# Kernel optimization log

Hardware: AMD Instinct MI355X
Metric: run time of the kernel (lower is better)

The kernel has to match this reference:

```python
import jax, jax.numpy as jnp
import numpy as np

B, LQ, LKV = 2, 2048, 2048
DQ, DKV, HID, NH = 1024, 1024, 1024, 16
HD = HID // NH
EPS = 1e-5


def setup_inputs() -> dict:
    key = jax.random.key(0)
    ks = jax.random.split(key, 12)
    s_q = 1.0 / np.sqrt(DQ)
    s_kv = 1.0 / np.sqrt(DKV)
    s_h = 1.0 / np.sqrt(HID)
    return {
        "query": jax.random.normal(ks[0], (B, LQ, DQ), jnp.float32),
        "key_value": jax.random.normal(ks[1], (B, LKV, DKV), jnp.float32),
        "Wq": jax.random.uniform(ks[2], (DQ, HID), jnp.float32, -s_q, s_q),
        "bq": jax.random.uniform(ks[3], (HID,), jnp.float32, -s_q, s_q),
        "Wk": jax.random.uniform(ks[4], (DKV, HID), jnp.float32, -s_kv, s_kv),
        "bk": jax.random.uniform(ks[5], (HID,), jnp.float32, -s_kv, s_kv),
        "Wv": jax.random.uniform(ks[6], (DKV, HID), jnp.float32, -s_kv, s_kv),
        "bv": jax.random.uniform(ks[7], (HID,), jnp.float32, -s_kv, s_kv),
        "Wo": jax.random.uniform(ks[8], (HID, DQ), jnp.float32, -s_h, s_h),
        "bo": jax.random.uniform(ks[9], (DQ,), jnp.float32, -s_h, s_h),
        "ln_gamma": jnp.ones((DQ,), jnp.float32),
        "ln_beta": jnp.zeros((DQ,), jnp.float32),
    }


def reference(query, key_value, Wq, bq, Wk, bk, Wv, bv, Wo, bo, ln_gamma, ln_beta):
    b, lq, _ = query.shape
    lkv = key_value.shape[1]
    # projections -> [b, heads, len, head_dim]
    Q = (query @ Wq + bq).reshape(b, lq, NH, HD).transpose(0, 2, 1, 3)
    K = (key_value @ Wk + bk).reshape(b, lkv, NH, HD).transpose(0, 2, 1, 3)
    V = (key_value @ Wv + bv).reshape(b, lkv, NH, HD).transpose(0, 2, 1, 3)
    scores = jnp.einsum("bhqd,bhkd->bhqk", Q, K) / jnp.sqrt(jnp.float32(HD))
    attn = jax.nn.softmax(scores, axis=-1)
    ctx = jnp.einsum("bhqk,bhkd->bhqd", attn, V)
    ctx = ctx.transpose(0, 2, 1, 3).reshape(b, lq, HID)
    out = ctx @ Wo + bo
    x = query + out
    mu = jnp.mean(x, axis=-1, keepdims=True)
    var = jnp.mean(jnp.square(x - mu), axis=-1, keepdims=True)
    return (x - mu) / jnp.sqrt(var + EPS) * ln_gamma + ln_beta
```

## Files before the change

kernel.cpp:

```cpp
#include <hip/hip_runtime.h>

typedef unsigned short u16;
typedef __bf16 bf16x8 __attribute__((ext_vector_type(8)));
typedef float f32x4 __attribute__((ext_vector_type(4)));
typedef unsigned short u16x4 __attribute__((ext_vector_type(4)));

#define LOG2E 1.44269504088896340736f
#define LDK 1040
#define LDV 2080
#define EXPM16 12599160.0f

__device__ __forceinline__ u16 f2bf(float f) {
  unsigned u = __float_as_uint(f);
  u += 0x7FFFu + ((u >> 16) & 1u);
  return (u16)(u >> 16);
}

__device__ __forceinline__ void load_lds16(const void* g, void* l) {
  __builtin_amdgcn_global_load_lds(
      (__attribute__((address_space(1))) void*)g,
      (__attribute__((address_space(3))) void*)l, 16, 0, 0);
}

__device__ __forceinline__ f32x4 mfma16(bf16x8 a, bf16x8 b, f32x4 c) {
  return __builtin_amdgcn_mfma_f32_16x16x32_bf16(a, b, c, 0, 0, 0);
}

__global__ __launch_bounds__(256) void pre_kernel(
    const float* __restrict__ q, const float* __restrict__ kv,
    u16* __restrict__ Xq, u16* __restrict__ Xkv,
    const float* __restrict__ Wq, const float* __restrict__ Wk,
    const float* __restrict__ Wv, const float* __restrict__ Wo,
    u16* __restrict__ Wqt, u16* __restrict__ Wkt,
    u16* __restrict__ Wvt, u16* __restrict__ Wot) {
  __shared__ float tile[32][33];
  const int bid = blockIdx.x;
  if (bid < 8192) {
    const int n4each = 4096 * 256;
    int i = bid * 256 + threadIdx.x;
    const float* src; u16* dst; int j;
    if (i < n4each) { src = q; dst = Xq; j = i; }
    else            { src = kv; dst = Xkv; j = i - n4each; }
    const float4 v = ((const float4*)src)[j];
    u16x4 o;
    o.x = f2bf(v.x); o.y = f2bf(v.y); o.z = f2bf(v.z); o.w = f2bf(v.w);
    ((u16x4*)dst)[j] = o;
    return;
  }
  const int t = bid - 8192;
  const int z = t >> 10, rem = t & 1023;
  const float* W; u16* Wt;
  switch (z) {
    case 0: W = Wq; Wt = Wqt; break;
    case 1: W = Wk; Wt = Wkt; break;
    case 2: W = Wv; Wt = Wvt; break;
    default: W = Wo; Wt = Wot; break;
  }
  const int tx = threadIdx.x & 31, ty = threadIdx.x >> 5;
  const int n0 = (rem & 31) * 32, k0 = (rem >> 5) * 32;
#pragma unroll
  for (int i = 0; i < 4; i++)
    tile[ty + i * 8][tx] = W[(size_t)(k0 + ty + i * 8) * 1024 + n0 + tx];
  __syncthreads();
#pragma unroll
  for (int i = 0; i < 4; i++)
    Wt[(size_t)(n0 + ty + i * 8) * 1024 + k0 + tx] = f2bf(tile[tx][ty + i * 8]);
}

__device__ __forceinline__ void gemm_tile(
    const u16* __restrict__ A, int lda, const u16* __restrict__ Bt, int ldb,
    const float* __restrict__ bias, bool brow, float scale,
    u16* __restrict__ Cb, float* __restrict__ Cf,
    int ldc, int bm, int bn, int K) {
  __shared__ alignas(16) u16 As[2][128 * 32];
  __shared__ alignas(16) u16 Bs[2][128 * 32];
  const int tid = threadIdx.x;
  const int wave = tid >> 6, lane = tid & 63;
  const int lm = lane & 15, kq = lane >> 4;
  const int g1 = tid, g2 = tid + 256;
  const u16* Ag1 = A + (size_t)(bm + (g1 >> 2)) * lda + (g1 & 3) * 8;
  const u16* Ag2 = A + (size_t)(bm + (g2 >> 2)) * lda + (g2 & 3) * 8;
  const u16* Bg1 = Bt + (size_t)(bn + (g1 >> 2)) * ldb + (g1 & 3) * 8;
  const u16* Bg2 = Bt + (size_t)(bn + (g2 >> 2)) * ldb + (g2 & 3) * 8;
  const int wm = (wave >> 1) * 64, wn = (wave & 1) * 64;

  load_lds16(Ag1, &As[0][g1 * 8]);
  load_lds16(Ag2, &As[0][g2 * 8]);
  load_lds16(Bg1, &Bs[0][g1 * 8]);
  load_lds16(Bg2, &Bs[0][g2 * 8]);

  f32x4 acc[4][4] = {};
  int cur = 0;
  for (int k0 = 0; k0 < K; k0 += 32) {
    if (k0 + 32 < K) {
      const int nxt = cur ^ 1;
      load_lds16(Ag1 + k0 + 32, &As[nxt][g1 * 8]);
      load_lds16(Ag2 + k0 + 32, &As[nxt][g2 * 8]);
      load_lds16(Bg1 + k0 + 32, &Bs[nxt][g1 * 8]);
      load_lds16(Bg2 + k0 + 32, &Bs[nxt][g2 * 8]);
      __builtin_amdgcn_sched_barrier(0);
      asm volatile("s_waitcnt vmcnt(4)" ::: "memory");
    } else {
      __builtin_amdgcn_sched_barrier(0);
      asm volatile("s_waitcnt vmcnt(0)" ::: "memory");
    }
    __builtin_amdgcn_sched_barrier(0);
    __builtin_amdgcn_s_barrier();

    __builtin_amdgcn_s_setprio(1);
    bf16x8 a[4], b[4];
#pragma unroll
    for (int t = 0; t < 4; t++)
      a[t] = *(const bf16x8*)&As[cur][(wm + t * 16 + lm) * 32 + kq * 8];
#pragma unroll
    for (int t = 0; t < 4; t++)
      b[t] = *(const bf16x8*)&Bs[cur][(wn + t * 16 + lm) * 32 + kq * 8];
#pragma unroll
    for (int mt = 0; mt < 4; mt++)
#pragma unroll
      for (int nt = 0; nt < 4; nt++)
        acc[mt][nt] = mfma16(a[mt], b[nt], acc[mt][nt]);
    __builtin_amdgcn_s_setprio(0);
    __builtin_amdgcn_sched_barrier(0);
    __builtin_amdgcn_s_barrier();
    cur ^= 1;
  }
#pragma unroll
  for (int mt = 0; mt < 4; mt++) {
    float rb[4];
#pragma unroll
    for (int r = 0; r < 4; r++)
      rb[r] = (bias && brow) ? bias[bm + wm + mt * 16 + kq * 4 + r] : 0.f;
#pragma unroll
    for (int nt = 0; nt < 4; nt++) {
      const int col = bn + wn + nt * 16 + lm;
      const float cb = (bias && !brow) ? bias[col] : 0.f;
#pragma unroll
      for (int r = 0; r < 4; r++) {
        const int row = bm + wm + mt * 16 + kq * 4 + r;
        const size_t idx = (size_t)row * ldc + col;
        const float v = (acc[mt][nt][r] + rb[r] + cb) * scale;
        if (Cf) Cf[idx] = v;
        else    Cb[idx] = f2bf(v);
      }
    }
  }
}

__global__ __launch_bounds__(256) void proj_gemm_kernel(
    const u16* __restrict__ Xq, const u16* __restrict__ Xkv,
    const u16* __restrict__ Wqt, const u16* __restrict__ Wkt, const u16* __restrict__ Wvt,
    const float* __restrict__ bq, const float* __restrict__ bk, const float* __restrict__ bv,
    u16* __restrict__ Qp, u16* __restrict__ Kp, u16* __restrict__ Vt, float qscale) {
  const int bid = blockIdx.x;
  const u16 *A, *Bt; const float* bias; u16* C;
  bool brow = false; float sc = 1.f; int ldc = 1024; int bm, bn;
  if (bid < 512) {
    const int r = bid & 255;
    const int xcd = r & 7, s = r >> 3;
    bm = (xcd * 4 + (s >> 3)) * 128;
    bn = (s & 7) * 128;
    if (bid < 256) { A = Xq;  Bt = Wqt; bias = bq; C = Qp; sc = qscale; }
    else           { A = Xkv; Bt = Wkt; bias = bk; C = Kp; ldc = LDK;  }
  } else {
    int r = bid - 512;
    const int z = r >> 7; r &= 127;
    const int xcd = r & 7, s = r >> 3;
    bm = (s >> 1) * 128;
    bn = (xcd * 2 + (s & 1)) * 128;
    A = Wvt; Bt = Xkv + (size_t)z * 2048 * 1024; bias = bv; brow = true;
    C = Vt + (size_t)z * 1024 * LDV; ldc = LDV;
  }
  gemm_tile(A, 1024, Bt, 1024, bias, brow, sc, C, nullptr, ldc, bm, bn, 1024);
}

__global__ __launch_bounds__(256) void ogemm_kernel(
    const u16* __restrict__ Ctx, const u16* __restrict__ Wot,
    float* __restrict__ X0, float* __restrict__ X1) {
  const int z = blockIdx.z;
  float* Cf = z ? X1 : X0;
  const int lin = blockIdx.x + 8 * blockIdx.y;
  const int xcd = lin & 7, s = lin >> 3;
  const int bm = (xcd * 4 + (s >> 3)) * 128, bn = (s & 7) * 128;
  gemm_tile(Ctx + z * 512, 1024, Wot + z * 512, 1024, nullptr, false, 1.f,
            nullptr, Cf, 1024, bm, bn, 512);
}

__global__ __launch_bounds__(512, 4) void attn_kernel(
    const u16* __restrict__ Qp, const u16* __restrict__ Kp,
    const u16* __restrict__ Vt, u16* __restrict__ ctx) {
  __shared__ alignas(16) u16 smem[32768];
  const int tid = threadIdx.x;
  const int wave = tid >> 6, lane = tid & 63;
  const int kh = wave >> 2, w4 = wave & 3;
  const int lm = lane & 15, kq = lane >> 4;
  const int L = blockIdx.x;
  const int xcd = L & 7, s = L >> 3;
  const int combo = xcd + 8 * (s >> 4);
  const int qb = s & 15;
  const int h = combo & 15, b = combo >> 4;
  const int qbase = qb * 128 + w4 * 32;

  u16* Ksh = smem + kh * 8192;
  u16* Vsh = smem + 16384 + kh * 8192;

  bf16x8 qf[2][2];
#pragma unroll
  for (int qt = 0; qt < 2; qt++)
#pragma unroll
    for (int kc = 0; kc < 2; kc++)
      qf[qt][kc] = *(const bf16x8*)(Qp + (size_t)(b * 2048 + qbase + qt * 16 + lm) * 1024 +
                                    h * 64 + kc * 32 + kq * 8);

  union { u16 u[8]; bf16x8 v; } uo;
#pragma unroll
  for (int i = 0; i < 8; i++) uo.u[i] = 0x3F80;
  const bf16x8 ones = uo.v;

  const u16* Kb = Kp + ((size_t)b * 2048 + kh * 1024) * LDK + h * 64;
  const u16* Vb = Vt + (size_t)(b * 1024 + h * 64) * LDV + kh * 1024;
  const int sp = lane ^ ((lane >> 3) & 7);
  const int c4 = sp >> 2, c3 = sp & 3;
  const int kvsw = ((lm * 4 + kq) ^ (lm >> 1)) * 8;

  f32x4 o[4][2] = {};
  f32x4 lsum[2] = {};

#pragma unroll
  for (int j = 0; j < 2; j++) {
    const int ii = w4 * 2 + j;
    const u16* gk = Kb + (size_t)(16 * (ii & 3) + c4) * LDK + (ii >> 2) * 32 + c3 * 8;
    load_lds16(gk, &Ksh[ii * 512 + lane * 8]);
    const u16* gv = Vb + (size_t)(16 * (ii & 3) + c4) * LDV + (ii >> 2) * 32 + c3 * 8;
    load_lds16(gv, &Vsh[ii * 512 + lane * 8]);
  }

  int cur = 0;
  for (int t = 0; t < 16; ++t) {
    if (t < 15) {
      const int kvn = (t + 1) * 64;
      const int nb = (cur ^ 1) * 4096;
#pragma unroll
      for (int j = 0; j < 2; j++) {
        const int ii = w4 * 2 + j;
        const u16* gk = Kb + (size_t)(kvn + 16 * (ii & 3) + c4) * LDK + (ii >> 2) * 32 + c3 * 8;
        load_lds16(gk, &Ksh[nb + ii * 512 + lane * 8]);
        const u16* gv = Vb + (size_t)(16 * (ii & 3) + c4) * LDV + kvn + (ii >> 2) * 32 + c3 * 8;
        load_lds16(gv, &Vsh[nb + ii * 512 + lane * 8]);
      }
      __builtin_amdgcn_sched_barrier(0);
      asm volatile("s_waitcnt vmcnt(4)" ::: "memory");
    } else {
      __builtin_amdgcn_sched_barrier(0);
      asm volatile("s_waitcnt vmcnt(0)" ::: "memory");
    }
    __builtin_amdgcn_sched_barrier(0);
    __builtin_amdgcn_s_barrier();

    const int cb = cur * 4096;
    __builtin_amdgcn_s_setprio(1);

    bf16x8 kf[2][4];
#pragma unroll
    for (int kc = 0; kc < 2; kc++)
#pragma unroll
      for (int kvt = 0; kvt < 4; kvt++)
        kf[kc][kvt] = *(const bf16x8*)&Ksh[cb + kc * 2048 + kvt * 512 + kvsw];

    bf16x8 pf[2][2];
#pragma unroll
    for (int qt = 0; qt < 2; qt++) {
      f32x4 st[4] = {};
#pragma unroll
      for (int kc = 0; kc < 2; kc++)
#pragma unroll
        for (int kvt = 0; kvt < 4; kvt++)
          st[kvt] = mfma16(kf[kc][kvt], qf[qt][kc], st[kvt]);
      unsigned Xd[4][2];
#pragma unroll
      for (int kvt = 0; kvt < 4; kvt++) {
        const unsigned e0 = __float_as_uint(fmaf(st[kvt][0], 128.f, EXPM16));
        const unsigned e1 = __float_as_uint(fmaf(st[kvt][1], 128.f, EXPM16));
        const unsigned e2 = __float_as_uint(fmaf(st[kvt][2], 128.f, EXPM16));
        const unsigned e3 = __float_as_uint(fmaf(st[kvt][3], 128.f, EXPM16));
        Xd[kvt][0] = __builtin_amdgcn_perm(e1, e0, 0x05040100u);
        Xd[kvt][1] = __builtin_amdgcn_perm(e3, e2, 0x05040100u);
      }
#pragma unroll
      for (int K1 = 0; K1 < 2; K1++) {
        unsigned a0 = Xd[2 * K1][0], b0 = Xd[2 * K1 + 1][0];
        unsigned a1 = Xd[2 * K1][1], b1 = Xd[2 * K1 + 1][1];
        asm("v_permlane32_swap_b32 %0, %1\n\t"
            "v_permlane16_swap_b32 %0, %1"
            : "+v"(a0), "+v"(b0));
        asm("v_permlane32_swap_b32 %0, %1\n\t"
            "v_permlane16_swap_b32 %0, %1"
            : "+v"(a1), "+v"(b1));
        union { uint4 u; bf16x8 v; } c;
        c.u.x = a0; c.u.y = a1; c.u.z = b0; c.u.w = b1;
        pf[qt][K1] = c.v;
      }
    }
#pragma unroll
    for (int s2 = 0; s2 < 2; s2++) {
      bf16x8 vf[4];
#pragma unroll
      for (int hdt = 0; hdt < 4; hdt++)
        vf[hdt] = *(const bf16x8*)&Vsh[cb + s2 * 2048 + hdt * 512 + kvsw];
#pragma unroll
      for (int qt = 0; qt < 2; qt++) {
        lsum[qt] = mfma16(ones, pf[qt][s2], lsum[qt]);
#pragma unroll
        for (int hdt = 0; hdt < 4; hdt++)
          o[hdt][qt] = mfma16(vf[hdt], pf[qt][s2], o[hdt][qt]);
      }
    }
    __builtin_amdgcn_s_setprio(0);
    __builtin_amdgcn_sched_barrier(0);
    __builtin_amdgcn_s_barrier();
    cur ^= 1;
  }

  __syncthreads();
  float* ex = (float*)smem;
  const int exi = (w4 * 64 + lane) * 36;
  if (kh == 1) {
#pragma unroll
    for (int qt = 0; qt < 2; qt++)
#pragma unroll
      for (int hdt = 0; hdt < 4; hdt++)
        *(f32x4*)&ex[exi + (qt * 4 + hdt) * 4] = o[hdt][qt];
    ex[exi + 32] = lsum[0][0];
    ex[exi + 33] = lsum[1][0];
  }
  __syncthreads();
  if (kh == 0) {
#pragma unroll
    for (int qt = 0; qt < 2; qt++) {
      const float lo = ex[exi + 32 + qt];
      const float rl = 1.f / (lsum[qt][0] + lo);
      u16* cbp = ctx + (size_t)(b * 2048 + qbase + qt * 16 + lm) * 1024 + h * 64 + kq * 4;
#pragma unroll
      for (int hdt = 0; hdt < 4; hdt++) {
        const f32x4 op = *(const f32x4*)&ex[exi + (qt * 4 + hdt) * 4];
        u16x4 w;
#pragma unroll
        for (int r = 0; r < 4; r++) w[r] = f2bf((o[hdt][qt][r] + op[r]) * rl);
        *(u16x4*)(cbp + hdt * 16) = w;
      }
    }
  }
}

__global__ __launch_bounds__(256) void ln_kernel(
    const float* __restrict__ x0, const float* __restrict__ x1,
    const float* __restrict__ q, const float* __restrict__ bo,
    const float* __restrict__ gamma, const float* __restrict__ beta,
    float* __restrict__ out) {
  const int row = blockIdx.x;
  const int t = threadIdx.x;
  const size_t g = (size_t)row * 256 + t;
  const float4 a = ((const float4*)x0)[g];
  const float4 c = ((const float4*)x1)[g];
  const float4 d = ((const float4*)q)[g];
  const float4 bv = ((const float4*)bo)[t];
  float4 v;
  v.x = a.x + c.x + d.x + bv.x;
  v.y = a.y + c.y + d.y + bv.y;
  v.z = a.z + c.z + d.z + bv.z;
  v.w = a.w + c.w + d.w + bv.w;
  float s = v.x + v.y + v.z + v.w;
  float s2 = v.x * v.x + v.y * v.y + v.z * v.z + v.w * v.w;
#pragma unroll
  for (int m = 1; m < 64; m <<= 1) {
    s += __shfl_xor(s, m);
    s2 += __shfl_xor(s2, m);
  }
  __shared__ float red[8];
  const int wave = t >> 6, lane = t & 63;
  if (lane == 0) { red[wave] = s; red[4 + wave] = s2; }
  __syncthreads();
  s = red[0] + red[1] + red[2] + red[3];
  s2 = red[4] + red[5] + red[6] + red[7];
  const float mu = s * (1.f / 1024.f);
  const float var = s2 * (1.f / 1024.f) - mu * mu;
  const float rstd = rsqrtf(var + 1e-5f);
  const float4 gm = ((const float4*)gamma)[t];
  const float4 bt = ((const float4*)beta)[t];
  float4 o;
  o.x = (v.x - mu) * rstd * gm.x + bt.x;
  o.y = (v.y - mu) * rstd * gm.y + bt.y;
  o.z = (v.z - mu) * rstd * gm.z + bt.z;
  o.w = (v.w - mu) * rstd * gm.w + bt.w;
  ((float4*)(out + (size_t)row * 1024))[t] = o;
}

extern "C" void kernel_launch(void* const* d_in, const int* in_sizes, int n_in,
                              void* d_out, int out_size, void* d_ws, size_t ws_size,
                              hipStream_t stream) {
  const float* query     = (const float*)d_in[0];
  const float* key_value = (const float*)d_in[1];
  const float* Wq = (const float*)d_in[2];
  const float* bq = (const float*)d_in[3];
  const float* Wk = (const float*)d_in[4];
  const float* bk = (const float*)d_in[5];
  const float* Wv = (const float*)d_in[6];
  const float* bv = (const float*)d_in[7];
  const float* Wo = (const float*)d_in[8];
  const float* bo = (const float*)d_in[9];
  const float* gamma = (const float*)d_in[10];
  const float* beta  = (const float*)d_in[11];
  float* out = (float*)d_out;

  const size_t MT = (size_t)4096 * 1024;
  const size_t WT = (size_t)1024 * 1024;
  char* ws = (char*)d_ws;
  u16* Xq  = (u16*)ws; ws += MT * 2;
  u16* Xkv = (u16*)ws; ws += MT * 2;
  u16* Wqt = (u16*)ws; ws += WT * 2;
  u16* Wkt = (u16*)ws; ws += WT * 2;
  u16* Wvt = (u16*)ws; ws += WT * 2;
  u16* Wot = (u16*)ws; ws += WT * 2;
  u16* Qp  = (u16*)ws; ws += MT * 2;
  u16* Kp  = (u16*)ws; ws += (size_t)4096 * LDK * 2;
  u16* Vt  = (u16*)ws; ws += (size_t)2048 * LDV * 2;
  float* X0 = (float*)ws; ws += MT * 4;
  float* X1 = (float*)ws; ws += MT * 4;
  u16* Ctx = Xq;

  const float qscale = 0.125f * LOG2E;

  pre_kernel<<<12288, 256, 0, stream>>>(query, key_value, Xq, Xkv,
                                        Wq, Wk, Wv, Wo, Wqt, Wkt, Wvt, Wot);
  proj_gemm_kernel<<<768, 256, 0, stream>>>(Xq, Xkv, Wqt, Wkt, Wvt, bq, bk, bv,
                                            Qp, Kp, Vt, qscale);
  attn_kernel<<<512, 512, 0, stream>>>(Qp, Kp, Vt, Ctx);
  ogemm_kernel<<<dim3(8, 32, 2), 256, 0, stream>>>(Ctx, Wot, X0, X1);
  ln_kernel<<<4096, 256, 0, stream>>>(X0, X1, query, bo, gamma, beta, out);
}
```

Before: 213.5 us.

## Swizzle GEMM LDS layout and replace split-K output GEMM with 64x128 tiles

The shared GEMM tile now loads global data into a swizzled LDS layout and reads it back with matching XOR-swizzled offsets, aimed at removing LDS bank conflicts on the MFMA fragment reads. The output projection drops its two-way split-K, which wrote two fp32 partial buffers. It becomes a dedicated kernel with 64x128 tiles over the full K=1024, 512 blocks, writing one buffer. The layernorm then reads one partial instead of two, cutting fp32 traffic at the cost of a longer K loop per block.

```diff
diff --git a/kernel.cpp b/kernel.cpp
--- a/kernel.cpp
+++ b/kernel.cpp
@@ -77,12 +77,15 @@
   const int tid = threadIdx.x;
   const int wave = tid >> 6, lane = tid & 63;
   const int lm = lane & 15, kq = lane >> 4;
+  const int sp = lane ^ ((lane >> 3) & 7);
+  const int r4 = sp >> 2, q3 = sp & 3;
   const int g1 = tid, g2 = tid + 256;
-  const u16* Ag1 = A + (size_t)(bm + (g1 >> 2)) * lda + (g1 & 3) * 8;
-  const u16* Ag2 = A + (size_t)(bm + (g2 >> 2)) * lda + (g2 & 3) * 8;
-  const u16* Bg1 = Bt + (size_t)(bn + (g1 >> 2)) * ldb + (g1 & 3) * 8;
-  const u16* Bg2 = Bt + (size_t)(bn + (g2 >> 2)) * ldb + (g2 & 3) * 8;
+  const u16* Ag1 = A + (size_t)(bm + wave * 16 + r4) * lda + q3 * 8;
+  const u16* Ag2 = A + (size_t)(bm + 64 + wave * 16 + r4) * lda + q3 * 8;
+  const u16* Bg1 = Bt + (size_t)(bn + wave * 16 + r4) * ldb + q3 * 8;
+  const u16* Bg2 = Bt + (size_t)(bn + 64 + wave * 16 + r4) * ldb + q3 * 8;
   const int wm = (wave >> 1) * 64, wn = (wave & 1) * 64;
+  const int kvsw = ((lm * 4 + kq) ^ (lm >> 1)) * 8;
 
   load_lds16(Ag1, &As[0][g1 * 8]);
   load_lds16(Ag2, &As[0][g2 * 8]);
@@ -111,10 +114,10 @@
     bf16x8 a[4], b[4];
 #pragma unroll
     for (int t = 0; t < 4; t++)
-      a[t] = *(const bf16x8*)&As[cur][(wm + t * 16 + lm) * 32 + kq * 8];
+      a[t] = *(const bf16x8*)&As[cur][((wm >> 4) + t) * 512 + kvsw];
 #pragma unroll
     for (int t = 0; t < 4; t++)
-      b[t] = *(const bf16x8*)&Bs[cur][(wn + t * 16 + lm) * 32 + kq * 8];
+      b[t] = *(const bf16x8*)&Bs[cur][((wn >> 4) + t) * 512 + kvsw];
 #pragma unroll
     for (int mt = 0; mt < 4; mt++)
 #pragma unroll
@@ -176,14 +179,75 @@
 
 __global__ __launch_bounds__(256) void ogemm_kernel(
     const u16* __restrict__ Ctx, const u16* __restrict__ Wot,
-    float* __restrict__ X0, float* __restrict__ X1) {
-  const int z = blockIdx.z;
-  float* Cf = z ? X1 : X0;
-  const int lin = blockIdx.x + 8 * blockIdx.y;
+    float* __restrict__ X) {
+  __shared__ alignas(16) u16 As[2][64 * 32];
+  __shared__ alignas(16) u16 Bs[2][128 * 32];
+  const int tid = threadIdx.x;
+  const int wave = tid >> 6, lane = tid & 63;
+  const int lm = lane & 15, kq = lane >> 4;
+  const int lin = blockIdx.x;
   const int xcd = lin & 7, s = lin >> 3;
-  const int bm = (xcd * 4 + (s >> 3)) * 128, bn = (s & 7) * 128;
-  gemm_tile(Ctx + z * 512, 1024, Wot + z * 512, 1024, nullptr, false, 1.f,
-            nullptr, Cf, 1024, bm, bn, 512);
+  const int bm = (xcd * 8 + (s >> 3)) * 64;
+  const int bn = (s & 7) * 128;
+  const int sp = lane ^ ((lane >> 3) & 7);
+  const int r4 = sp >> 2, q3 = sp & 3;
+  const int g1 = tid, g2 = tid + 256;
+  const u16* Ag  = Ctx + (size_t)(bm + wave * 16 + r4) * 1024 + q3 * 8;
+  const u16* Bg1 = Wot + (size_t)(bn + wave * 16 + r4) * 1024 + q3 * 8;
+  const u16* Bg2 = Wot + (size_t)(bn + 64 + wave * 16 + r4) * 1024 + q3 * 8;
+  const int wn = wave * 32;
+  const int kvsw = ((lm * 4 + kq) ^ (lm >> 1)) * 8;
+
+  load_lds16(Ag,  &As[0][g1 * 8]);
+  load_lds16(Bg1, &Bs[0][g1 * 8]);
+  load_lds16(Bg2, &Bs[0][g2 * 8]);
+
+  f32x4 acc[4][2] = {};
+  int cur = 0;
+  for (int k0 = 0; k0 < 1024; k0 += 32) {
+    if (k0 + 32 < 1024) {
+      const int nxt = cur ^ 1;
+      load_lds16(Ag + k0 + 32,  &As[nxt][g1 * 8]);
+      load_lds16(Bg1 + k0 + 32, &Bs[nxt][g1 * 8]);
+      load_lds16(Bg2 + k0 + 32, &Bs[nxt][g2 * 8]);
+      __builtin_amdgcn_sched_barrier(0);
+      asm volatile("s_waitcnt vmcnt(3)" ::: "memory");
+    } else {
+      __builtin_amdgcn_sched_barrier(0);
+      asm volatile("s_waitcnt vmcnt(0)" ::: "memory");
+    }
+    __builtin_amdgcn_sched_barrier(0);
+    __builtin_amdgcn_s_barrier();
+
+    __builtin_amdgcn_s_setprio(1);
+    bf16x8 a[4], b[2];
+#pragma unroll
+    for (int t = 0; t < 4; t++)
+      a[t] = *(const bf16x8*)&As[cur][t * 512 + kvsw];
+#pragma unroll
+    for (int t = 0; t < 2; t++)
+      b[t] = *(const bf16x8*)&Bs[cur][((wn >> 4) + t) * 512 + kvsw];
+#pragma unroll
+    for (int mt = 0; mt < 4; mt++)
+#pragma unroll
+      for (int nt = 0; nt < 2; nt++)
+        acc[mt][nt] = mfma16(a[mt], b[nt], acc[mt][nt]);
+    __builtin_amdgcn_s_setprio(0);
+    __builtin_amdgcn_sched_barrier(0);
+    __builtin_amdgcn_s_barrier();
+    cur ^= 1;
+  }
+#pragma unroll
+  for (int mt = 0; mt < 4; mt++)
+#pragma unroll
+    for (int nt = 0; nt < 2; nt++) {
+      const int col = bn + wn + nt * 16 + lm;
+#pragma unroll
+      for (int r = 0; r < 4; r++) {
+        const int row = bm + mt * 16 + kq * 4 + r;
+        X[(size_t)row * 1024 + col] = acc[mt][nt][r];
+      }
+    }
 }
 
 __global__ __launch_bounds__(512, 4) void attn_kernel(
@@ -353,7 +417,7 @@
 }
 
 __global__ __launch_bounds__(256) void ln_kernel(
-    const float* __restrict__ x0, const float* __restrict__ x1,
+    const float* __restrict__ x0,
     const float* __restrict__ q, const float* __restrict__ bo,
     const float* __restrict__ gamma, const float* __restrict__ beta,
     float* __restrict__ out) {
@@ -361,14 +425,13 @@
   const int t = threadIdx.x;
   const size_t g = (size_t)row * 256 + t;
   const float4 a = ((const float4*)x0)[g];
-  const float4 c = ((const float4*)x1)[g];
   const float4 d = ((const float4*)q)[g];
   const float4 bv = ((const float4*)bo)[t];
   float4 v;
-  v.x = a.x + c.x + d.x + bv.x;
-  v.y = a.y + c.y + d.y + bv.y;
-  v.z = a.z + c.z + d.z + bv.z;
-  v.w = a.w + c.w + d.w + bv.w;
+  v.x = a.x + d.x + bv.x;
+  v.y = a.y + d.y + bv.y;
+  v.z = a.z + d.z + bv.z;
+  v.w = a.w + d.w + bv.w;
   float s = v.x + v.y + v.z + v.w;
   float s2 = v.x * v.x + v.y * v.y + v.z * v.z + v.w * v.w;
 #pragma unroll
@@ -425,7 +488,6 @@
   u16* Kp  = (u16*)ws; ws += (size_t)4096 * LDK * 2;
   u16* Vt  = (u16*)ws; ws += (size_t)2048 * LDV * 2;
   float* X0 = (float*)ws; ws += MT * 4;
-  float* X1 = (float*)ws; ws += MT * 4;
   u16* Ctx = Xq;
 
   const float qscale = 0.125f * LOG2E;
@@ -435,6 +497,6 @@
   proj_gemm_kernel<<<768, 256, 0, stream>>>(Xq, Xkv, Wqt, Wkt, Wvt, bq, bk, bv,
                                             Qp, Kp, Vt, qscale);
   attn_kernel<<<512, 512, 0, stream>>>(Qp, Kp, Vt, Ctx);
-  ogemm_kernel<<<dim3(8, 32, 2), 256, 0, stream>>>(Ctx, Wot, X0, X1);
-  ln_kernel<<<4096, 256, 0, stream>>>(X0, X1, query, bo, gamma, beta, out);
-}
+  ogemm_kernel<<<512, 256, 0, stream>>>(Ctx, Wot, X0);
+  ln_kernel<<<4096, 256, 0, stream>>>(X0, query, bo, gamma, beta, out);
+}
```

Result: slower. 225.9 us (+5.8%).
